# Kernel optimization log

Hardware: AMD Instinct MI355X
Metric: run time of the kernel (lower is better)

## Reference

```python
import jax, jax.numpy as jnp
import numpy as np

DIM = 96       # d_model / channels
DSTATE = 16    # SSM state size N
DINNER = 2 * DIM   # expand=2 -> 192
DTRANK = 6     # ceil(DIM/16)
K = 4          # scan directions
B, H, W = 2, 56, 56


def _ln(x, g, b, eps=1e-5):
    m = x.mean(-1, keepdims=True)
    v = x.var(-1, keepdims=True)
    return (x - m) * jax.lax.rsqrt(v + eps) * g + b


def _dwconv3(x, w, b):  # x [B,C,H,W], w [C,1,3,3] depthwise, SAME padding
    y = jax.lax.conv_general_dilated(x, w, (1, 1), [(1, 1), (1, 1)],
                                     feature_group_count=x.shape[1],
                                     dimension_numbers=('NCHW', 'OIHW', 'NCHW'))
    return y + b[None, :, None, None]


def _bn(x, g, b, m, v, eps=1e-5):  # eval-mode BatchNorm2d on NCHW
    inv = jax.lax.rsqrt(v + eps)
    return (x - m[None, :, None, None]) * (inv * g)[None, :, None, None] + b[None, :, None, None]


def _selective_scan(u, dt, A, Bs, Cs, Dp, dt_bias):
    # u, dt: [B,K,D,L]; A: [K,D,N]; Bs,Cs: [B,K,N,L]; Dp, dt_bias: [K,D]
    dt = jax.nn.softplus(dt + dt_bias[None, :, :, None])
    dA = jnp.exp(jnp.einsum('bkdl,kdn->lbkdn', dt, A))           # [L,B,K,D,N]
    dBu = jnp.einsum('bkdl,bknl,bkdl->lbkdn', dt, Bs, u)          # [L,B,K,D,N]
    Ct = jnp.moveaxis(Cs, -1, 0)                                  # [L,B,K,N]
    h0 = jnp.zeros(dA.shape[1:], dA.dtype)

    def step(h, inp):
        dA_l, dBu_l, C_l = inp
        h = dA_l * h + dBu_l
        return h, jnp.einsum('bkdn,bkn->bkd', h, C_l)

    _, ys = jax.lax.scan(step, h0, (dA, dBu, Ct))                 # ys [L,B,K,D]
    return jnp.moveaxis(ys, 0, -1) + u * Dp[None, :, :, None]     # [B,K,D,L]


def setup_inputs() -> dict:
    key = jax.random.key(0)
    ks = jax.random.split(key, 12)
    s = 0.02
    f32 = jnp.float32
    inp = {}
    inp['x'] = jax.random.normal(ks[0], (B, H, W, DIM), f32)
    # conv branch: depthwise 3x3 + BN + ReLU + 1x1 + BN
    inp['dw_w'] = jax.random.normal(ks[1], (DIM, 1, 3, 3), f32) * s
    inp['dw_b'] = jnp.zeros((DIM,), f32)
    inp['bn1_g'] = jnp.ones((DIM,), f32); inp['bn1_b'] = jnp.zeros((DIM,), f32)
    inp['bn1_m'] = jnp.zeros((DIM,), f32); inp['bn1_v'] = jnp.ones((DIM,), f32)
    inp['pw_w'] = jax.random.normal(ks[2], (DIM, DIM), f32) * s
    inp['pw_b'] = jnp.zeros((DIM,), f32)
    inp['bn2_g'] = jnp.ones((DIM,), f32); inp['bn2_b'] = jnp.zeros((DIM,), f32)
    inp['bn2_m'] = jnp.zeros((DIM,), f32); inp['bn2_v'] = jnp.ones((DIM,), f32)
    # pre-mamba LayerNorm
    inp['ln_g'] = jnp.ones((DIM,), f32); inp['ln_b'] = jnp.zeros((DIM,), f32)
    # SS2D params
    inp['in_proj_w'] = jax.random.normal(ks[3], (2 * DINNER, DIM), f32) * s
    inp['conv_w'] = jax.random.normal(ks[4], (DINNER, 1, 3, 3), f32) * s
    inp['conv_b'] = jnp.zeros((DINNER,), f32)
    inp['x_proj_w'] = jax.random.normal(ks[5], (K, DTRANK + 2 * DSTATE, DINNER), f32) * s
    inp['dt_w'] = jax.random.normal(ks[6], (K, DINNER, DTRANK), f32) * s
    inp['dt_b'] = jnp.full((K, DINNER), -4.6, f32)  # softplus(dt_b) ~= 0.01
    inp['A_logs'] = jnp.log(jnp.tile(jnp.arange(1, DSTATE + 1, dtype=f32), (K * DINNER, 1)))
    inp['Ds'] = jnp.ones((K * DINNER,), f32)
    inp['out_norm_g'] = jnp.ones((DINNER,), f32); inp['out_norm_b'] = jnp.zeros((DINNER,), f32)
    inp['out_proj_w'] = jax.random.normal(ks[7], (DIM, DINNER), f32) * s
    # fusion: Linear(2*dim, dim) + LayerNorm(dim)
    inp['fus_w'] = jax.random.normal(ks[8], (DIM, 2 * DIM), f32) * s
    inp['fus_b'] = jnp.zeros((DIM,), f32)
    inp['fus_ln_g'] = jnp.ones((DIM,), f32); inp['fus_ln_b'] = jnp.zeros((DIM,), f32)
    return inp


def reference(x, dw_w, dw_b, bn1_g, bn1_b, bn1_m, bn1_v, pw_w, pw_b,
              bn2_g, bn2_b, bn2_m, bn2_v, ln_g, ln_b,
              in_proj_w, conv_w, conv_b, x_proj_w, dt_w, dt_b, A_logs, Ds,
              out_norm_g, out_norm_b, out_proj_w, fus_w, fus_b, fus_ln_g, fus_ln_b):
    Bsz, Hh, Ww, C = x.shape
    L = Hh * Ww
    # ----- conv branch -----
    xc = jnp.transpose(x, (0, 3, 1, 2))                       # [B,C,H,W]
    c = jax.nn.relu(_bn(_dwconv3(xc, dw_w, dw_b), bn1_g, bn1_b, bn1_m, bn1_v))
    c = jnp.einsum('bchw,oc->bohw', c, pw_w) + pw_b[None, :, None, None]
    conv_out = jnp.transpose(_bn(c, bn2_g, bn2_b, bn2_m, bn2_v), (0, 2, 3, 1))
    # ----- mamba (SS2D) branch -----
    xn = _ln(x, ln_g, ln_b)
    xz = xn @ in_proj_w.T                                     # [B,H,W,2*Din]
    xm, z = jnp.split(xz, 2, axis=-1)
    xm = jnp.transpose(xm, (0, 3, 1, 2))                      # [B,Din,H,W]
    xm = jax.nn.silu(_dwconv3(xm, conv_w, conv_b))
    v1 = xm.reshape(Bsz, DINNER, L)                           # row-major scan
    v2 = jnp.transpose(xm, (0, 1, 3, 2)).reshape(Bsz, DINNER, L)  # col-major scan
    xs = jnp.stack([v1, v2, v1[..., ::-1], v2[..., ::-1]], axis=1)  # [B,4,Din,L]
    x_dbl = jnp.einsum('bkdl,kcd->bkcl', xs, x_proj_w)
    dts, Bmat, Cmat = jnp.split(x_dbl, [DTRANK, DTRANK + DSTATE], axis=2)
    dts = jnp.einsum('bkrl,kdr->bkdl', dts, dt_w)
    A = -jnp.exp(A_logs).reshape(K, DINNER, DSTATE)
    out_y = _selective_scan(xs, dts, A, Bmat, Cmat, Ds.reshape(K, DINNER), dt_b)
    y1 = out_y[:, 0]
    inv_y = out_y[:, 2:4][..., ::-1]
    y2 = inv_y[:, 0]
    y3 = jnp.transpose(inv_y[:, 1].reshape(Bsz, DINNER, Ww, Hh), (0, 1, 3, 2)).reshape(Bsz, DINNER, L)
    y4 = jnp.transpose(out_y[:, 1].reshape(Bsz, DINNER, Ww, Hh), (0, 1, 3, 2)).reshape(Bsz, DINNER, L)
    y = jnp.transpose(y1 + y2 + y3 + y4, (0, 2, 1)).reshape(Bsz, Hh, Ww, DINNER)
    y = _ln(y, out_norm_g, out_norm_b)
    y = y * jax.nn.silu(z)
    mamba_out = y @ out_proj_w.T                              # [B,H,W,C]
    # ----- fusion + residual -----
    fused = jnp.concatenate([conv_out, mamba_out], axis=-1) @ fus_w.T + fus_b
    fused = _ln(fused, fus_ln_g, fus_ln_b)
    return x + fused
```

## Files before the change

kernel.cpp:

```cpp
#include <hip/hip_runtime.h>
#include <math.h>

#define BZ 2
#define HH 56
#define WW 56
#define LL 3136
#define CC 96
#define DI 192
#define NS 16
#define RR 6
#define NT 49
#define NCH 98
#define CH 32

#define OFF_CONV   0
#define OFF_XMRAW  602112
#define OFF_Z      1806336
#define OFF_V1     3010560
#define OFF_V2     4214784
#define OFF_DT     5419008
#define OFF_BS     10235904
#define OFF_CS     10637312
#define OFF_Y      11038720
#define OFF_Y13    15855616
#define OFF_T      18264064
#define OFF_W2     19468288

__device__ __forceinline__ float softplusf(float x) {
    if (x > 20.f) return x;
    return log1pf(__expf(x));
}

__global__ __launch_bounds__(256) void k0_prep(const float* __restrict__ fus_w,
                                               const float* __restrict__ opw,
                                               const float* __restrict__ A_logs,
                                               float* __restrict__ W2,
                                               float* __restrict__ negA) {
    int i = blockIdx.x * 256 + threadIdx.x;
    if (i < CC * DI) {
        int o = i / DI, d = i % DI;
        float acc = 0.f;
        for (int j = 0; j < CC; ++j)
            acc += fus_w[o * DI + CC + j] * opw[j * DI + d];
        W2[i] = acc;
    } else if (i < CC * DI + 4 * DI * NS) {
        int j = i - CC * DI;
        negA[j] = -__expf(A_logs[j]);
    }
}

__global__ __launch_bounds__(256) void k1a_dw(const float* __restrict__ x,
    const float* __restrict__ dw_w, const float* __restrict__ dw_b,
    const float* __restrict__ bn1_g, const float* __restrict__ bn1_b,
    const float* __restrict__ bn1_m, const float* __restrict__ bn1_v,
    float* __restrict__ cbuf) {
    int i = blockIdx.x * 256 + threadIdx.x;
    if (i >= BZ * LL * CC) return;
    int c = i % CC;
    int bl = i / CC;
    int l = bl % LL, b = bl / LL;
    int h = l / WW, w = l % WW;
    float acc = dw_b[c];
    #pragma unroll
    for (int dy = -1; dy <= 1; ++dy) {
        int hh = h + dy; if (hh < 0 || hh >= HH) continue;
        #pragma unroll
        for (int dx = -1; dx <= 1; ++dx) {
            int ww = w + dx; if (ww < 0 || ww >= WW) continue;
            acc += x[((b * HH + hh) * WW + ww) * CC + c] * dw_w[c * 9 + (dy + 1) * 3 + (dx + 1)];
        }
    }
    float inv = rsqrtf(bn1_v[c] + 1e-5f);
    float v = (acc - bn1_m[c]) * inv * bn1_g[c] + bn1_b[c];
    cbuf[i] = fmaxf(v, 0.f);
}

__global__ __launch_bounds__(256) void k1b_pw(const float* __restrict__ cbuf,
    const float* __restrict__ pw_w, const float* __restrict__ pw_b,
    const float* __restrict__ bn2_g, const float* __restrict__ bn2_b,
    const float* __restrict__ bn2_m, const float* __restrict__ bn2_v,
    float* __restrict__ conv_out) {
    int t0 = blockIdx.x * 64;
    int og = blockIdx.y;
    int b = blockIdx.z;
    int lane = threadIdx.x & 63;
    int wvu = __builtin_amdgcn_readfirstlane(threadIdx.x >> 6);
    __shared__ float ct[CC * 65];
    __shared__ float res[64 * 25];
    const float* cb = cbuf + (b * LL + t0) * CC;
    for (int e = threadIdx.x; e < 64 * CC; e += 256) {
        int p = e / CC, c = e % CC;
        ct[c * 65 + p] = cb[e];
    }
    __syncthreads();
    int o0 = og * 24 + wvu * 6;
    float acc[6];
    const float* pb = pw_b + o0;
    #pragma unroll
    for (int j = 0; j < 6; ++j) acc[j] = pb[j];
    const float* wb = pw_w + o0 * CC;
    for (int c = 0; c < CC; ++c) {
        float xv = ct[c * 65 + lane];
        #pragma unroll
        for (int j = 0; j < 6; ++j)
            acc[j] += xv * wb[j * CC + c];
    }
    #pragma unroll
    for (int j = 0; j < 6; ++j) {
        int o = o0 + j;
        float inv = rsqrtf(bn2_v[o] + 1e-5f);
        res[lane * 25 + wvu * 6 + j] = (acc[j] - bn2_m[o]) * inv * bn2_g[o] + bn2_b[o];
    }
    __syncthreads();
    float* ob = conv_out + (b * LL + t0) * CC + og * 24;
    for (int e = threadIdx.x; e < 64 * 24; e += 256) {
        int pl = e / 24, o = e % 24;
        ob[pl * CC + o] = res[pl * 25 + o];
    }
}

__global__ __launch_bounds__(256) void k2_inproj(const float* __restrict__ x,
    const float* __restrict__ ln_g, const float* __restrict__ ln_b,
    const float* __restrict__ ipw,
    float* __restrict__ xm_raw, float* __restrict__ z_buf) {
    int t0 = blockIdx.x * 64;
    int og = blockIdx.y;
    int b = blockIdx.z;
    int lane = threadIdx.x & 63;
    int wv = threadIdx.x >> 6;
    int wvu = __builtin_amdgcn_readfirstlane(wv);
    __shared__ float xt[64 * 97];
    __shared__ float xn[96 * 65];
    __shared__ float ps[4][64], ps2[4][64];
    const float* xb = x + (b * LL + t0) * CC;
    for (int e = threadIdx.x; e < 64 * CC; e += 256) {
        int p = e / CC, c = e % CC;
        xt[p * 97 + c] = xb[e];
    }
    __syncthreads();
    float s = 0.f, s2 = 0.f;
    #pragma unroll
    for (int j = 0; j < 24; ++j) {
        float v = xt[lane * 97 + wvu * 24 + j];
        s += v; s2 += v * v;
    }
    ps[wv][lane] = s; ps2[wv][lane] = s2;
    __syncthreads();
    float st = 0.f, st2 = 0.f;
    #pragma unroll
    for (int i = 0; i < 4; ++i) { st += ps[i][lane]; st2 += ps2[i][lane]; }
    float m = st * (1.f / 96.f);
    float inv = rsqrtf(st2 * (1.f / 96.f) - m * m + 1e-5f);
    #pragma unroll
    for (int j = 0; j < 24; ++j) {
        int c = wvu * 24 + j;
        xn[c * 65 + lane] = (xt[lane * 97 + c] - m) * inv * ln_g[c] + ln_b[c];
    }
    __syncthreads();
    float acc[12];
    #pragma unroll
    for (int j = 0; j < 12; ++j) acc[j] = 0.f;
    int o0 = og * 48 + wvu * 12;
    const float* wbase = ipw + o0 * CC;
    for (int c = 0; c < CC; ++c) {
        float xv = xn[c * 65 + lane];
        #pragma unroll
        for (int j = 0; j < 12; ++j)
            acc[j] += xv * wbase[j * CC + c];
    }
    int p = t0 + lane;
    #pragma unroll
    for (int j = 0; j < 12; ++j) {
        int out = o0 + j;
        if (out < DI) xm_raw[(b * DI + out) * LL + p] = acc[j];
        else          z_buf[(b * DI + (out - DI)) * LL + p] = acc[j];
    }
}

__global__ __launch_bounds__(256) void k3_dw(const float* __restrict__ xm_raw,
    const float* __restrict__ conv_w, const float* __restrict__ conv_b,
    float* __restrict__ v1, float* __restrict__ v2) {
    int bd = blockIdx.x;
    int half = blockIdx.y;
    int d = bd % DI;
    int h0 = half * 28;
    __shared__ float tile[28 * 57];
    const float* src = xm_raw + bd * LL;
    float wloc[9];
    #pragma unroll
    for (int i = 0; i < 9; ++i) wloc[i] = conv_w[d * 9 + i];
    float bias = conv_b[d];
    for (int e = threadIdx.x; e < 28 * WW; e += 256) {
        int hl = e / WW, w = e % WW;
        int h = h0 + hl;
        float acc = bias;
        #pragma unroll
        for (int dy = -1; dy <= 1; ++dy) {
            int hh = h + dy; if (hh < 0 || hh >= HH) continue;
            #pragma unroll
            for (int dx = -1; dx <= 1; ++dx) {
                int ww = w + dx; if (ww < 0 || ww >= WW) continue;
                acc += src[hh * WW + ww] * wloc[(dy + 1) * 3 + (dx + 1)];
            }
        }
        float sig = 1.f / (1.f + __expf(-acc));
        float v = acc * sig;
        v1[bd * LL + h * WW + w] = v;
        tile[hl * 57 + w] = v;
    }
    __syncthreads();
    for (int e = threadIdx.x; e < 28 * WW; e += 256) {
        int w = e / 28, hl = e % 28;
        v2[bd * LL + w * HH + h0 + hl] = tile[hl * 57 + w];
    }
}

__global__ __launch_bounds__(256) void k4a_xproj(const float* __restrict__ v1,
    const float* __restrict__ v2, const float* __restrict__ xpw,
    float* __restrict__ dtr_g, float* __restrict__ B_s, float* __restrict__ C_s) {
    int tile = blockIdx.x;
    int k = blockIdx.y, b = blockIdx.z;
    int lane = threadIdx.x & 63;
    int wvu = __builtin_amdgcn_readfirstlane(threadIdx.x >> 6);
    int t0 = tile * 64;
    int r0 = wvu * 10; if (r0 > 28) r0 = 28;
    const float* src = ((k & 1) == 0 ? v1 : v2) + b * DI * LL + t0;
    float acc[10];
    #pragma unroll
    for (int i = 0; i < 10; ++i) acc[i] = 0.f;
    const float* wbase = xpw + (k * 38 + r0) * DI;
    for (int d = 0; d < DI; ++d) {
        float xv = src[d * LL + lane];
        #pragma unroll
        for (int i = 0; i < 10; ++i)
            acc[i] += xv * wbase[i * DI + d];
    }
    int bk = b * 4 + k;
    int p = t0 + lane;
    #pragma unroll
    for (int i = 0; i < 10; ++i) {
        int c = r0 + i;
        if (c < RR) {
            dtr_g[(bk * RR + c) * LL + p] = acc[i];
        } else if (c < RR + NS) {
            B_s[(bk * NS + (c - RR)) * LL + p] = acc[i];
        } else {
            C_s[(bk * NS + (c - RR - NS)) * LL + p] = acc[i];
        }
    }
}

__global__ __launch_bounds__(256) void k4b_dt(const float* __restrict__ dtr_g,
    const float* __restrict__ dtw, const float* __restrict__ dtb,
    float* __restrict__ dt_s) {
    int t0 = blockIdx.x * 64;
    int k = blockIdx.y, b = blockIdx.z;
    int lane = threadIdx.x & 63;
    int wvu = __builtin_amdgcn_readfirstlane(threadIdx.x >> 6);
    int bk = b * 4 + k;
    int p = t0 + lane;
    float r[RR];
    #pragma unroll
    for (int i = 0; i < RR; ++i) r[i] = dtr_g[(bk * RR + i) * LL + p];
    for (int i = 0; i < 48; ++i) {
        int d = wvu * 48 + i;
        float a = dtb[k * DI + d];
        const float* wr = dtw + (k * DI + d) * RR;
        #pragma unroll
        for (int q = 0; q < RR; ++q)
            a += r[q] * wr[q];
        dt_s[(bk * DI + d) * LL + p] = softplusf(a);
    }
}

__global__ __launch_bounds__(128, 4) void k5a_scan(const float* __restrict__ dt_s,
    const float* __restrict__ B_s, const float* __restrict__ C_s,
    const float* __restrict__ v1, const float* __restrict__ v2,
    const float* __restrict__ A_logs, float* __restrict__ y_scan,
    float* __restrict__ hl_buf, float* __restrict__ Tbuf) {
    int bx = blockIdx.x;
    int dg = bx % 3, c = bx / 3;
    int k = blockIdx.y, b = blockIdx.z;
    int bk = b * 4 + k;
    int tid = threadIdx.x;
    int lane = tid & 63;
    int wvu = __builtin_amdgcn_readfirstlane(tid >> 6);
    int d0 = dg * 64, d = d0 + lane;
    bool fwd = (k < 2);
    int s0 = fwd ? c * CH : (LL - (c + 1) * CH);
    __shared__ float dtl[64 * 32];
    __shared__ float ul[64 * 32];
    __shared__ alignas(16) float bc[32 * 32];
    float Ae[8];
    const float* ap = A_logs + (k * DI + d) * NS + wvu * 8;
    #pragma unroll
    for (int n = 0; n < 8; ++n) Ae[n] = -__expf(ap[n]) * 1.442695040888963f;
    const float* dtp = dt_s + (bk * DI + d0) * LL + s0;
    const float* up  = ((k & 1) == 0 ? v1 : v2) + (b * DI + d0) * LL + s0;
    #pragma unroll
    for (int q = 0; q < 4; ++q) {
        int e = q * 128 + tid;
        int row = e >> 3;
        int p4 = (e & 7) << 2;
        float4 dv = *(const float4*)(dtp + row * LL + p4);
        float4 uv = *(const float4*)(up + row * LL + p4);
        float dvv[4] = {dv.x, dv.y, dv.z, dv.w};
        float uvv[4] = {uv.x, uv.y, uv.z, uv.w};
        int rsw = row & 31;
        #pragma unroll
        for (int t = 0; t < 4; ++t) {
            int s = fwd ? (p4 + t) : (31 - (p4 + t));
            dtl[row * 32 + (s ^ rsw)] = dvv[t];
            ul [row * 32 + (s ^ rsw)] = dvv[t] * uvv[t];
        }
    }
    #pragma unroll
    for (int q = 0; q < 2; ++q) {
        int e = q * 128 + tid;
        int row = e >> 3;
        int p4 = (e & 7) << 2;
        const float* src = (row < 16 ? B_s + (bk * NS + row) * LL
                                     : C_s + (bk * NS + (row - 16)) * LL) + s0 + p4;
        float4 v = *(const float4*)src;
        float vv[4] = {v.x, v.y, v.z, v.w};
        #pragma unroll
        for (int t = 0; t < 4; ++t) {
            int s = fwd ? (p4 + t) : (31 - (p4 + t));
            bc[s * 32 + (row ^ ((s & 7) << 2))] = vv[t];
        }
    }
    __syncthreads();
    float h[8];
    #pragma unroll
    for (int n = 0; n < 8; ++n) h[n] = 0.f;
    float cum = 0.f;
    int lbase = lane * 32;
    int lsw = lane & 31;
    int w8 = wvu * 8;
    #pragma unroll
    for (int seg = 0; seg < 4; ++seg) {
        float yv_[8];
        #pragma unroll
        for (int jj = 0; jj < 8; ++jj) {
            int j = seg * 8 + jj;
            float dtv = dtl[lbase + (j ^ lsw)];
            float du  = ul [lbase + (j ^ lsw)];
            cum += dtv;
            int cswz = (j & 7) << 2;
            const float* rb0 = &bc[j * 32 + ( w8       ^ cswz)];
            const float* rb1 = &bc[j * 32 + ((w8 +  4) ^ cswz)];
            const float* rc0 = &bc[j * 32 + ((w8 + 16) ^ cswz)];
            const float* rc1 = &bc[j * 32 + ((w8 + 20) ^ cswz)];
            float4 b0 = *(const float4*)rb0, b1 = *(const float4*)rb1;
            float4 c0 = *(const float4*)rc0, c1 = *(const float4*)rc1;
            float bv[8] = {b0.x, b0.y, b0.z, b0.w, b1.x, b1.y, b1.z, b1.w};
            float cv[8] = {c0.x, c0.y, c0.z, c0.w, c1.x, c1.y, c1.z, c1.w};
            float y = 0.f;
            #pragma unroll
            for (int n = 0; n < 8; ++n) {
                h[n] = exp2f(dtv * Ae[n]) * h[n] + du * bv[n];
                y += h[n] * cv[n];
            }
            yv_[jj] = y;
        }
        __syncthreads();
        float* dst = (wvu == 0) ? dtl : ul;
        #pragma unroll
        for (int jj = 0; jj < 8; ++jj) {
            int j = seg * 8 + jj;
            dst[lbase + (j ^ lsw)] = yv_[jj];
        }
    }
    __syncthreads();
    float* yp = y_scan + (bk * DI + d0) * LL + s0;
    #pragma unroll
    for (int q = 0; q < 4; ++q) {
        int e = q * 128 + tid;
        int row = e >> 3;
        int p4 = (e & 7) << 2;
        int rsw = row & 31;
        float ov[4];
        #pragma unroll
        for (int t = 0; t < 4; ++t) {
            int s = fwd ? (p4 + t) : (31 - (p4 + t));
            ov[t] = dtl[row * 32 + (s ^ rsw)] + ul[row * 32 + (s ^ rsw)];
        }
        *(float4*)(yp + row * LL + p4) = make_float4(ov[0], ov[1], ov[2], ov[3]);
    }
    float4* hp4 = (float4*)(hl_buf + (bk * NCH + c) * (DI * NS) + d * NS + wvu * 8);
    hp4[0] = make_float4(h[0], h[1], h[2], h[3]);
    hp4[1] = make_float4(h[4], h[5], h[6], h[7]);
    if (wvu == 0) Tbuf[(bk * NCH + c) * DI + d] = cum;
}

__global__ __launch_bounds__(64) void k5c_comb(float* __restrict__ hl_buf,
    const float* __restrict__ Tbuf, const float* __restrict__ negA) {
    int dg = blockIdx.x, k = blockIdx.y, b = blockIdx.z;
    int lane = threadIdx.x, dl = lane >> 4, n = lane & 15;
    int d = dg * 4 + dl;
    int bk = b * 4 + k;
    const int HS = DI * NS;
    float Av = negA[(k * DI + d) * NS + n];
    float* hp = hl_buf + (bk * NCH) * HS + dg * 64 + lane;
    const float* Tp = Tbuf + (bk * NCH) * DI + d;
    float hl[8], T[8];
    #pragma unroll
    for (int i = 0; i < 8; ++i) { hl[i] = hp[i * HS]; T[i] = Tp[i * DI]; }
    float H = 0.f;
    for (int cb = 0; cb < 96; cb += 8) {
        #pragma unroll
        for (int i = 0; i < 8; ++i) {
            int c = cb + i;
            float hlv = hl[i], Tv = T[i];
            int nc = c + 8;
            if (nc < NCH) { hl[i] = hp[nc * HS]; T[i] = Tp[nc * DI]; }
            hp[c * HS] = H;
            H = hlv + __expf(Av * Tv) * H;
        }
    }
    hp[96 * HS] = H;
    H = hl[0] + __expf(Av * T[0]) * H;
    hp[97 * HS] = H;
}

__global__ __launch_bounds__(256) void k5d_corr(const float* __restrict__ dtr_g,
    const float* __restrict__ dtw, const float* __restrict__ dtb,
    const float* __restrict__ C_s, const float* __restrict__ hin,
    const float* __restrict__ negA, float* __restrict__ y_scan) {
    int t  = blockIdx.x % (NCH - 1);
    int ds = blockIdx.x / (NCH - 1);
    int k = blockIdx.y, b = blockIdx.z;
    bool fwd = (k < 2);
    int c  = fwd ? (t + 1) : (NCH - 1 - t);
    int s0 = fwd ? (t + 1) * CH : t * CH;
    int p32 = threadIdx.x & 31, sl = threadIdx.x >> 5;
    int bk = b * 4 + k;
    __shared__ float c_l[16 * 33];
    for (int e = threadIdx.x; e < 16 * CH; e += 256) {
        int n = e >> 5, s = e & 31;
        c_l[n * 33 + s] = C_s[(bk * NS + n) * LL + s0 + s];
    }
    const float* rp = dtr_g + (bk * RR) * LL + s0 + p32;
    float r[RR];
    #pragma unroll
    for (int q = 0; q < RR; ++q) r[q] = rp[q * LL];
    __syncthreads();
    for (int j = 0; j < 6; ++j) {
        int d = ds * 48 + sl * 6 + j;
        int dd = k * DI + d;
        const float* wr = dtw + dd * RR;
        float a = dtb[dd];
        #pragma unroll
        for (int q = 0; q < RR; ++q)
            a += r[q] * wr[q];
        float dtv = softplusf(a);
        float cum = dtv;
        if (fwd) {
            #pragma unroll
            for (int off = 1; off < 32; off <<= 1) {
                float o = __shfl_up(cum, off, 32);
                if (p32 >= off) cum += o;
            }
        } else {
            #pragma unroll
            for (int off = 1; off < 32; off <<= 1) {
                float o = __shfl_down(cum, off, 32);
                if (p32 < 32 - off) cum += o;
            }
        }
        const float* hp = hin + (bk * NCH + c) * (DI * NS) + d * 16;
        const float* ap = negA + (k * DI + d) * NS;
        float4 h0 = *(const float4*)(hp);
        float4 h1 = *(const float4*)(hp + 4);
        float4 h2 = *(const float4*)(hp + 8);
        float4 h3 = *(const float4*)(hp + 12);
        float4 a0 = *(const float4*)(ap);
        float4 a1 = *(const float4*)(ap + 4);
        float4 a2 = *(const float4*)(ap + 8);
        float4 a3 = *(const float4*)(ap + 12);
        float hv[16] = {h0.x, h0.y, h0.z, h0.w, h1.x, h1.y, h1.z, h1.w,
                        h2.x, h2.y, h2.z, h2.w, h3.x, h3.y, h3.z, h3.w};
        float av[16] = {a0.x, a0.y, a0.z, a0.w, a1.x, a1.y, a1.z, a1.w,
                        a2.x, a2.y, a2.z, a2.w, a3.x, a3.y, a3.z, a3.w};
        float acc = 0.f;
        #pragma unroll
        for (int n = 0; n < 16; ++n) {
            acc += c_l[n * 33 + p32] * __expf(av[n] * cum) * hv[n];
        }
        y_scan[(bk * DI + d) * LL + s0 + p32] += acc;
    }
}

__global__ __launch_bounds__(256) void k5b_tr(const float* __restrict__ y_scan,
                                              float* __restrict__ y13t) {
    int idx = blockIdx.x;
    int d = idx % DI;
    int bk = idx / DI;
    int kk = bk % 2, b = bk / 2;
    int k = (kk == 0) ? 1 : 3;
    __shared__ float tile[HH * 57];
    const float* src = y_scan + ((b * 4 + k) * DI + d) * LL;
    for (int e = threadIdx.x; e < LL; e += 256) {
        int w = e / HH, h = e % HH;
        tile[h * 57 + w] = src[e];
    }
    __syncthreads();
    float* dst = y13t + idx * LL;
    for (int e = threadIdx.x; e < LL; e += 256) {
        int h = e / WW, w = e % WW;
        dst[e] = tile[h * 57 + w];
    }
}

__global__ __launch_bounds__(256) void k6_gather(const float* __restrict__ y_scan,
    const float* __restrict__ y13t, const float* __restrict__ v1,
    const float* __restrict__ z_buf, const float* __restrict__ Ds,
    const float* __restrict__ ong, const float* __restrict__ onb,
    float* __restrict__ t_buf) {
    int t0 = blockIdx.x * 16;
    int b = blockIdx.y;
    int p16 = threadIdx.x & 15, sl = threadIdx.x >> 4;
    int p = t0 + p16;
    __shared__ float yv[DI * 17];
    __shared__ float ps[16][16], ps2[16][16];
    float s = 0.f, s2 = 0.f;
    for (int j = 0; j < 12; ++j) {
        int d = sl * 12 + j;
        float dsum = Ds[d] + Ds[DI + d] + Ds[2 * DI + d] + Ds[3 * DI + d];
        float val = y_scan[((b * 4 + 0) * DI + d) * LL + p]
                  + y_scan[((b * 4 + 2) * DI + d) * LL + p]
                  + y13t[((b * 2 + 0) * DI + d) * LL + p]
                  + y13t[((b * 2 + 1) * DI + d) * LL + p]
                  + v1[(b * DI + d) * LL + p] * dsum;
        yv[d * 17 + p16] = val;
        s += val; s2 += val * val;
    }
    ps[sl][p16] = s; ps2[sl][p16] = s2;
    __syncthreads();
    float st = 0.f, st2 = 0.f;
    #pragma unroll
    for (int i = 0; i < 16; ++i) { st += ps[i][p16]; st2 += ps2[i][p16]; }
    float m = st * (1.f / 192.f);
    float inv = rsqrtf(st2 * (1.f / 192.f) - m * m + 1e-5f);
    for (int j = 0; j < 12; ++j) {
        int d = sl * 12 + j;
        float val = (yv[d * 17 + p16] - m) * inv * ong[d] + onb[d];
        float zz = z_buf[(b * DI + d) * LL + p];
        float sig = 1.f / (1.f + __expf(-zz));
        t_buf[(b * DI + d) * LL + p] = val * zz * sig;
    }
}

__global__ __launch_bounds__(256) void k7a_mm(const float* __restrict__ t_buf,
    const float* __restrict__ conv_out, const float* __restrict__ W2,
    const float* __restrict__ fus_w, const float* __restrict__ fus_b,
    float* __restrict__ fusedT) {
    int t0 = blockIdx.x * 64;
    int og = blockIdx.y;
    int b = blockIdx.z;
    int lane = threadIdx.x & 63;
    int wvu = __builtin_amdgcn_readfirstlane(threadIdx.x >> 6);
    __shared__ float ct[CC * 65];
    const float* cb = conv_out + (b * LL + t0) * CC;
    for (int e = threadIdx.x; e < 64 * CC; e += 256) {
        int p = e / CC, c = e % CC;
        ct[c * 65 + p] = cb[e];
    }
    __syncthreads();
    int o0 = og * 12 + wvu * 3;
    float acc[3];
    #pragma unroll
    for (int j = 0; j < 3; ++j) acc[j] = fus_b[o0 + j];
    int p = t0 + lane;
    const float* w2 = W2 + o0 * DI;
    for (int d = 0; d < DI; ++d) {
        float tv = t_buf[(b * DI + d) * LL + p];
        #pragma unroll
        for (int j = 0; j < 3; ++j)
            acc[j] += tv * w2[j * DI + d];
    }
    const float* fw = fus_w + o0 * DI;
    for (int c = 0; c < CC; ++c) {
        float cv = ct[c * 65 + lane];
        #pragma unroll
        for (int j = 0; j < 3; ++j)
            acc[j] += cv * fw[j * DI + c];
    }
    #pragma unroll
    for (int j = 0; j < 3; ++j)
        fusedT[(b * CC + o0 + j) * LL + p] = acc[j];
}

__global__ __launch_bounds__(256) void k7b_ln(const float* __restrict__ fusedT,
    const float* __restrict__ flg, const float* __restrict__ flb,
    const float* __restrict__ x, float* __restrict__ out) {
    int t0 = blockIdx.x * 16;
    int b = blockIdx.y;
    int p16 = threadIdx.x & 15, sl = threadIdx.x >> 4;
    __shared__ float ft[CC * 17];
    __shared__ float res[16 * 97];
    __shared__ float ps[16][16], ps2[16][16];
    for (int e = threadIdx.x; e < CC * 16; e += 256) {
        int o = e >> 4, p = e & 15;
        ft[o * 17 + p] = fusedT[(b * CC + o) * LL + t0 + p];
    }
    __syncthreads();
    float s = 0.f, s2 = 0.f;
    #pragma unroll
    for (int j = 0; j < 6; ++j) {
        float v = ft[(sl * 6 + j) * 17 + p16];
        s += v; s2 += v * v;
    }
    ps[sl][p16] = s; ps2[sl][p16] = s2;
    __syncthreads();
    float st = 0.f, st2 = 0.f;
    #pragma unroll
    for (int i = 0; i < 16; ++i) { st += ps[i][p16]; st2 += ps2[i][p16]; }
    float m = st * (1.f / 96.f);
    float inv = rsqrtf(st2 * (1.f / 96.f) - m * m + 1e-5f);
    #pragma unroll
    for (int j = 0; j < 6; ++j) {
        int o = sl * 6 + j;
        res[p16 * 97 + o] = (ft[o * 17 + p16] - m) * inv * flg[o] + flb[o];
    }
    __syncthreads();
    const float* xb = x + (b * LL + t0) * CC;
    float* ob = out + (b * LL + t0) * CC;
    for (int e = threadIdx.x; e < 16 * CC; e += 256) {
        int pl = e / CC, o = e % CC;
        ob[e] = xb[e] + res[pl * 97 + o];
    }
}

extern "C" void kernel_launch(void* const* d_in, const int* in_sizes, int n_in,
                              void* d_out, int out_size, void* d_ws, size_t ws_size,
                              hipStream_t stream) {
    const float* x        = (const float*)d_in[0];
    const float* dw_w     = (const float*)d_in[1];
    const float* dw_b     = (const float*)d_in[2];
    const float* bn1_g    = (const float*)d_in[3];
    const float* bn1_b    = (const float*)d_in[4];
    const float* bn1_m    = (const float*)d_in[5];
    const float* bn1_v    = (const float*)d_in[6];
    const float* pw_w     = (const float*)d_in[7];
    const float* pw_b     = (const float*)d_in[8];
    const float* bn2_g    = (const float*)d_in[9];
    const float* bn2_b    = (const float*)d_in[10];
    const float* bn2_m    = (const float*)d_in[11];
    const float* bn2_v    = (const float*)d_in[12];
    const float* ln_g     = (const float*)d_in[13];
    const float* ln_b     = (const float*)d_in[14];
    const float* ipw      = (const float*)d_in[15];
    const float* conv_w   = (const float*)d_in[16];
    const float* conv_b   = (const float*)d_in[17];
    const float* xpw      = (const float*)d_in[18];
    const float* dtw      = (const float*)d_in[19];
    const float* dtb      = (const float*)d_in[20];
    const float* A_logs   = (const float*)d_in[21];
    const float* Ds       = (const float*)d_in[22];
    const float* ong      = (const float*)d_in[23];
    const float* onb      = (const float*)d_in[24];
    const float* opw      = (const float*)d_in[25];
    const float* fus_w    = (const float*)d_in[26];
    const float* fus_b    = (const float*)d_in[27];
    const float* flg      = (const float*)d_in[28];
    const float* flb      = (const float*)d_in[29];

    float* ws = (float*)d_ws;
    float* conv_out = ws + OFF_CONV;
    float* xm_raw   = ws + OFF_XMRAW;
    float* z_buf    = ws + OFF_Z;
    float* v1       = ws + OFF_V1;
    float* v2       = ws + OFF_V2;
    float* dt_s     = ws + OFF_DT;
    float* B_s      = ws + OFF_BS;
    float* C_s      = ws + OFF_CS;
    float* y_scan   = ws + OFF_Y;
    float* y13t     = ws + OFF_Y13;
    float* t_buf    = ws + OFF_T;
    float* W2       = ws + OFF_W2;
    float* cbuf     = y13t;
    float* hl_buf   = y13t;
    float* Tbuf     = xm_raw;
    float* dtr_g    = xm_raw + 262144;
    float* negA     = t_buf;
    float* fusedT   = y13t;
    float* out      = (float*)d_out;

    k0_prep<<<dim3((CC * DI + 4 * DI * NS + 255) / 256), dim3(256), 0, stream>>>(
        fus_w, opw, A_logs, W2, negA);
    k1a_dw<<<dim3((BZ * LL * CC + 255) / 256), dim3(256), 0, stream>>>(x, dw_w, dw_b,
                                                     bn1_g, bn1_b, bn1_m, bn1_v, cbuf);
    k1b_pw<<<dim3(NT, 4, BZ), dim3(256), 0, stream>>>(cbuf, pw_w, pw_b,
                                                   bn2_g, bn2_b, bn2_m, bn2_v, conv_out);
    k2_inproj<<<dim3(NT, 8, BZ), dim3(256), 0, stream>>>(x, ln_g, ln_b, ipw, xm_raw, z_buf);
    k3_dw<<<dim3(BZ * DI, 2), dim3(256), 0, stream>>>(xm_raw, conv_w, conv_b, v1, v2);
    k4a_xproj<<<dim3(NT, 4, BZ), dim3(256), 0, stream>>>(v1, v2, xpw, dtr_g, B_s, C_s);
    k4b_dt<<<dim3(NT, 4, BZ), dim3(256), 0, stream>>>(dtr_g, dtw, dtb, dt_s);
    k5a_scan<<<dim3(3 * NCH, 4, BZ), dim3(128), 0, stream>>>(dt_s, B_s, C_s, v1, v2, A_logs,
                                                             y_scan, hl_buf, Tbuf);
    k5c_comb<<<dim3(48, 4, BZ), dim3(64), 0, stream>>>(hl_buf, Tbuf, negA);
    k5d_corr<<<dim3((NCH - 1) * 4, 4, BZ), dim3(256), 0, stream>>>(dtr_g, dtw, dtb, C_s,
                                                             hl_buf, negA, y_scan);
    k5b_tr<<<dim3(BZ * 2 * DI), dim3(256), 0, stream>>>(y_scan, y13t);
    k6_gather<<<dim3(196, BZ), dim3(256), 0, stream>>>(y_scan, y13t, v1, z_buf, Ds, ong, onb, t_buf);
    k7a_mm<<<dim3(NT, 8, BZ), dim3(256), 0, stream>>>(t_buf, conv_out, W2, fus_w, fus_b, fusedT);
    k7b_ln<<<dim3(196, BZ), dim3(256), 0, stream>>>(fusedT, flg, flb, x, out);
}
```

Measured before the change: 350.6 us.

## Fuse transpose, gather/LN, fusion matmul and final LN into one kernel

```diff
diff --git a/kernel.cpp b/kernel.cpp
--- a/kernel.cpp
+++ b/kernel.cpp
@@ -491,46 +491,38 @@
     }
 }
 
-__global__ __launch_bounds__(256) void k5b_tr(const float* __restrict__ y_scan,
-                                              float* __restrict__ y13t) {
-    int idx = blockIdx.x;
-    int d = idx % DI;
-    int bk = idx / DI;
-    int kk = bk % 2, b = bk / 2;
-    int k = (kk == 0) ? 1 : 3;
-    __shared__ float tile[HH * 57];
-    const float* src = y_scan + ((b * 4 + k) * DI + d) * LL;
-    for (int e = threadIdx.x; e < LL; e += 256) {
-        int w = e / HH, h = e % HH;
-        tile[h * 57 + w] = src[e];
-    }
-    __syncthreads();
-    float* dst = y13t + idx * LL;
-    for (int e = threadIdx.x; e < LL; e += 256) {
-        int h = e / WW, w = e % WW;
-        dst[e] = tile[h * 57 + w];
-    }
-}
-
-__global__ __launch_bounds__(256) void k6_gather(const float* __restrict__ y_scan,
-    const float* __restrict__ y13t, const float* __restrict__ v1,
-    const float* __restrict__ z_buf, const float* __restrict__ Ds,
-    const float* __restrict__ ong, const float* __restrict__ onb,
-    float* __restrict__ t_buf) {
+__global__ __launch_bounds__(256) void k6_fused(const float* __restrict__ y_scan,
+    const float* __restrict__ v1, const float* __restrict__ z_buf,
+    const float* __restrict__ Ds, const float* __restrict__ ong,
+    const float* __restrict__ onb, const float* __restrict__ W2,
+    const float* __restrict__ fus_w, const float* __restrict__ fus_b,
+    const float* __restrict__ flg, const float* __restrict__ flb,
+    const float* __restrict__ conv_out, const float* __restrict__ x,
+    float* __restrict__ out) {
     int t0 = blockIdx.x * 16;
     int b = blockIdx.y;
-    int p16 = threadIdx.x & 15, sl = threadIdx.x >> 4;
+    int tid = threadIdx.x;
+    int p16 = tid & 15, sl = tid >> 4;
     int p = t0 + p16;
+    int hh = p / WW, ww2 = p % WW;
+    int tp = ww2 * HH + hh;
     __shared__ float yv[DI * 17];
+    __shared__ float ct[CC * 17];
+    __shared__ float res[16 * 97];
     __shared__ float ps[16][16], ps2[16][16];
+    const float* cb = conv_out + (b * LL + t0) * CC;
+    for (int e = tid; e < 16 * CC; e += 256) {
+        int pp = e / CC, c = e % CC;
+        ct[c * 17 + pp] = cb[e];
+    }
     float s = 0.f, s2 = 0.f;
     for (int j = 0; j < 12; ++j) {
         int d = sl * 12 + j;
         float dsum = Ds[d] + Ds[DI + d] + Ds[2 * DI + d] + Ds[3 * DI + d];
         float val = y_scan[((b * 4 + 0) * DI + d) * LL + p]
                   + y_scan[((b * 4 + 2) * DI + d) * LL + p]
-                  + y13t[((b * 2 + 0) * DI + d) * LL + p]
-                  + y13t[((b * 2 + 1) * DI + d) * LL + p]
+                  + y_scan[((b * 4 + 1) * DI + d) * LL + tp]
+                  + y_scan[((b * 4 + 3) * DI + d) * LL + tp]
                   + v1[(b * DI + d) * LL + p] * dsum;
         yv[d * 17 + p16] = val;
         s += val; s2 += val * val;
@@ -547,86 +539,46 @@
         float val = (yv[d * 17 + p16] - m) * inv * ong[d] + onb[d];
         float zz = z_buf[(b * DI + d) * LL + p];
         float sig = 1.f / (1.f + __expf(-zz));
-        t_buf[(b * DI + d) * LL + p] = val * zz * sig;
-    }
-}
-
-__global__ __launch_bounds__(256) void k7a_mm(const float* __restrict__ t_buf,
-    const float* __restrict__ conv_out, const float* __restrict__ W2,
-    const float* __restrict__ fus_w, const float* __restrict__ fus_b,
-    float* __restrict__ fusedT) {
-    int t0 = blockIdx.x * 64;
-    int og = blockIdx.y;
-    int b = blockIdx.z;
-    int lane = threadIdx.x & 63;
-    int wvu = __builtin_amdgcn_readfirstlane(threadIdx.x >> 6);
-    __shared__ float ct[CC * 65];
-    const float* cb = conv_out + (b * LL + t0) * CC;
-    for (int e = threadIdx.x; e < 64 * CC; e += 256) {
-        int p = e / CC, c = e % CC;
-        ct[c * 65 + p] = cb[e];
-    }
-    __syncthreads();
-    int o0 = og * 12 + wvu * 3;
-    float acc[3];
-    #pragma unroll
-    for (int j = 0; j < 3; ++j) acc[j] = fus_b[o0 + j];
-    int p = t0 + lane;
+        yv[d * 17 + p16] = val * zz * sig;
+    }
+    __syncthreads();
+    int o0 = sl * 6;
+    float acc[6];
+    #pragma unroll
+    for (int j = 0; j < 6; ++j) acc[j] = fus_b[o0 + j];
     const float* w2 = W2 + o0 * DI;
     for (int d = 0; d < DI; ++d) {
-        float tv = t_buf[(b * DI + d) * LL + p];
-        #pragma unroll
-        for (int j = 0; j < 3; ++j)
+        float tv = yv[d * 17 + p16];
+        #pragma unroll
+        for (int j = 0; j < 6; ++j)
             acc[j] += tv * w2[j * DI + d];
     }
     const float* fw = fus_w + o0 * DI;
     for (int c = 0; c < CC; ++c) {
-        float cv = ct[c * 65 + lane];
-        #pragma unroll
-        for (int j = 0; j < 3; ++j)
+        float cv = ct[c * 17 + p16];
+        #pragma unroll
+        for (int j = 0; j < 6; ++j)
             acc[j] += cv * fw[j * DI + c];
     }
-    #pragma unroll
-    for (int j = 0; j < 3; ++j)
-        fusedT[(b * CC + o0 + j) * LL + p] = acc[j];
-}
-
-__global__ __launch_bounds__(256) void k7b_ln(const float* __restrict__ fusedT,
-    const float* __restrict__ flg, const float* __restrict__ flb,
-    const float* __restrict__ x, float* __restrict__ out) {
-    int t0 = blockIdx.x * 16;
-    int b = blockIdx.y;
-    int p16 = threadIdx.x & 15, sl = threadIdx.x >> 4;
-    __shared__ float ft[CC * 17];
-    __shared__ float res[16 * 97];
-    __shared__ float ps[16][16], ps2[16][16];
-    for (int e = threadIdx.x; e < CC * 16; e += 256) {
-        int o = e >> 4, p = e & 15;
-        ft[o * 17 + p] = fusedT[(b * CC + o) * LL + t0 + p];
-    }
-    __syncthreads();
-    float s = 0.f, s2 = 0.f;
+    float fs = 0.f, fs2 = 0.f;
+    #pragma unroll
+    for (int j = 0; j < 6; ++j) { fs += acc[j]; fs2 += acc[j] * acc[j]; }
+    ps[sl][p16] = fs; ps2[sl][p16] = fs2;
+    __syncthreads();
+    float fst = 0.f, fst2 = 0.f;
+    #pragma unroll
+    for (int i = 0; i < 16; ++i) { fst += ps[i][p16]; fst2 += ps2[i][p16]; }
+    float fm = fst * (1.f / 96.f);
+    float finv = rsqrtf(fst2 * (1.f / 96.f) - fm * fm + 1e-5f);
     #pragma unroll
     for (int j = 0; j < 6; ++j) {
-        float v = ft[(sl * 6 + j) * 17 + p16];
-        s += v; s2 += v * v;
-    }
-    ps[sl][p16] = s; ps2[sl][p16] = s2;
-    __syncthreads();
-    float st = 0.f, st2 = 0.f;
-    #pragma unroll
-    for (int i = 0; i < 16; ++i) { st += ps[i][p16]; st2 += ps2[i][p16]; }
-    float m = st * (1.f / 96.f);
-    float inv = rsqrtf(st2 * (1.f / 96.f) - m * m + 1e-5f);
-    #pragma unroll
-    for (int j = 0; j < 6; ++j) {
-        int o = sl * 6 + j;
-        res[p16 * 97 + o] = (ft[o * 17 + p16] - m) * inv * flg[o] + flb[o];
+        int o = o0 + j;
+        res[p16 * 97 + o] = (acc[j] - fm) * finv * flg[o] + flb[o];
     }
     __syncthreads();
     const float* xb = x + (b * LL + t0) * CC;
     float* ob = out + (b * LL + t0) * CC;
-    for (int e = threadIdx.x; e < 16 * CC; e += 256) {
+    for (int e = tid; e < 16 * CC; e += 256) {
         int pl = e / CC, o = e % CC;
         ob[e] = xb[e] + res[pl * 97 + o];
     }
@@ -677,14 +629,12 @@
     float* C_s      = ws + OFF_CS;
     float* y_scan   = ws + OFF_Y;
     float* y13t     = ws + OFF_Y13;
-    float* t_buf    = ws + OFF_T;
     float* W2       = ws + OFF_W2;
     float* cbuf     = y13t;
     float* hl_buf   = y13t;
     float* Tbuf     = xm_raw;
     float* dtr_g    = xm_raw + 262144;
-    float* negA     = t_buf;
-    float* fusedT   = y13t;
+    float* negA     = ws + OFF_T;
     float* out      = (float*)d_out;
 
     k0_prep<<<dim3((CC * DI + 4 * DI * NS + 255) / 256), dim3(256), 0, stream>>>(
@@ -702,8 +652,7 @@
     k5c_comb<<<dim3(48, 4, BZ), dim3(64), 0, stream>>>(hl_buf, Tbuf, negA);
     k5d_corr<<<dim3((NCH - 1) * 4, 4, BZ), dim3(256), 0, stream>>>(dtr_g, dtw, dtb, C_s,
                                                              hl_buf, negA, y_scan);
-    k5b_tr<<<dim3(BZ * 2 * DI), dim3(256), 0, stream>>>(y_scan, y13t);
-    k6_gather<<<dim3(196, BZ), dim3(256), 0, stream>>>(y_scan, y13t, v1, z_buf, Ds, ong, onb, t_buf);
-    k7a_mm<<<dim3(NT, 8, BZ), dim3(256), 0, stream>>>(t_buf, conv_out, W2, fus_w, fus_b, fusedT);
-    k7b_ln<<<dim3(196, BZ), dim3(256), 0, stream>>>(fusedT, flg, flb, x, out);
-}
+    k6_fused<<<dim3(196, BZ), dim3(256), 0, stream>>>(y_scan, v1, z_buf, Ds, ong, onb,
+                                                      W2, fus_w, fus_b, flg, flb,
+                                                      conv_out, x, out);
+}
```

After: 368.4 us. 5.1% more time.
